# Kernel optimization log

Measured on AMD Instinct MI355X. Metric: run time of the kernel, lower is better.

Reference implementation:

```python
import jax, jax.numpy as jnp
import numpy as np

W_BIT = 4
OUT_F = 11008
IN_F = 4096
K = 16


def unpack_sign(q_bytes):
    """q_bytes: [n_bytes] int32 holding uint8 values. Little-endian bit order.
    Returns float32 signs in {-1, +1} of shape [OUT_F, IN_F]."""
    bits = (q_bytes[:, None] >> jnp.arange(8, dtype=q_bytes.dtype)) & 1  # [n_bytes, 8]
    signs = (2 * bits - 1).astype(jnp.float32)
    return signs.reshape(OUT_F, IN_F)


def setup_inputs() -> dict:
    key = jax.random.key(0)
    k0, k1, k2, k3 = jax.random.split(key, 4)
    x = jax.random.normal(k0, (4, 2048, IN_F), dtype=jnp.float32)
    # packed sign bits: one byte stores 8 signs; OUT_F*IN_F//8 bytes per bit-plane
    qweight = jax.random.randint(k1, (W_BIT, OUT_F * IN_F // 8), 0, 256, dtype=jnp.int32)
    u = jax.random.normal(k2, (W_BIT, OUT_F, K), dtype=jnp.float32) * 0.05
    vt = jax.random.normal(k3, (W_BIT, K, IN_F), dtype=jnp.float32) * 0.05
    return {"x": x, "qweight": qweight, "u": u, "vt": vt}


def reference(x, qweight, u, vt):
    # Reconstruct full weight: w = sum_i sign_i * (u_i @ vt_i), then GEMM x @ w.T.
    # Loop over the small fixed w_bit count to avoid holding all [OUT,IN] bit-planes at once.
    w = jnp.zeros((OUT_F, IN_F), dtype=x.dtype)
    for i in range(W_BIT):
        signs = unpack_sign(qweight[i])            # [OUT_F, IN_F]
        w = w + signs * (u[i] @ vt[i])             # rank-K reconstruction masked by signs
    return x @ w.T                                  # [B, S, OUT_F]
```

## Files before the change

### kernel.cpp

```cpp
#include <hip/hip_runtime.h>
#include <hip/hip_bf16.h>

#define W_BIT 4
#define OUT_F 11008
#define IN_F 4096
#define KRANK 16
#define M_DIM 8192
#define QW_PLANE (OUT_F * IN_F / 8)

#define N_DIM OUT_F
#define K_DIM IN_F
#define NT 64
#define NBN 43

typedef __attribute__((ext_vector_type(8))) short short8;
typedef __attribute__((ext_vector_type(4))) float f32x4;

__device__ __forceinline__ short f2bf(float f) {
    union { float f; unsigned u; } v;
    v.f = f;
    unsigned r = v.u + 0x7fffu + ((v.u >> 16) & 1u);
    return (short)(r >> 16);
}

__device__ __forceinline__ void async16(void* lds, const void* g) {
    __builtin_amdgcn_global_load_lds(
        (const __attribute__((address_space(1))) unsigned int*)g,
        (__attribute__((address_space(3))) unsigned int*)lds,
        16, 0, 0);
}

#define BAR() __builtin_amdgcn_s_barrier()
#define SBAR0() __builtin_amdgcn_sched_barrier(0)
#define LGKM(n) do { asm volatile("s_waitcnt lgkmcnt(" #n ")" ::: "memory"); \
                     __builtin_amdgcn_sched_barrier(0); } while (0)
#define VMC(n) do { asm volatile("s_waitcnt vmcnt(" #n ")" ::: "memory"); \
                    __builtin_amdgcn_sched_barrier(0); } while (0)
#define PRIO1() __builtin_amdgcn_s_setprio(1)
#define PRIO0() __builtin_amdgcn_s_setprio(0)

__global__ __launch_bounds__(256) void convert_x_kernel(
    const float* __restrict__ x, short* __restrict__ xb) {
    int tid = blockIdx.x * blockDim.x + threadIdx.x;
    int stride = gridDim.x * blockDim.x;
    const int n8 = (M_DIM * IN_F) / 8;
    for (int i = tid; i < n8; i += stride) {
        f32x4 a = ((const f32x4*)x)[2 * i];
        f32x4 b = ((const f32x4*)x)[2 * i + 1];
        short8 o;
        o[0] = f2bf(a[0]); o[1] = f2bf(a[1]); o[2] = f2bf(a[2]); o[3] = f2bf(a[3]);
        o[4] = f2bf(b[0]); o[5] = f2bf(b[1]); o[6] = f2bf(b[2]); o[7] = f2bf(b[3]);
        ((short8*)xb)[i] = o;
    }
}

__global__ __launch_bounds__(256) void reconstruct_w_kernel(
    const int* __restrict__ qw, const float* __restrict__ u,
    const float* __restrict__ vt, short* __restrict__ wb) {
    __shared__ float vts[W_BIT][KRANK][128];
    __shared__ float us[W_BIT][KRANK][64];

    const int t = threadIdx.x;
    const int o0 = blockIdx.y * 64;
    const int c0 = blockIdx.x * 128;

    for (int idx = t; idx < W_BIT * KRANK * 128; idx += 256) {
        int i = idx >> 11;
        int rem = idx & 2047;
        int k = rem >> 7;
        int c = rem & 127;
        vts[i][k][c] = vt[(i * KRANK + k) * IN_F + c0 + c];
    }
    for (int idx = t; idx < W_BIT * KRANK * 64; idx += 256) {
        int i = idx >> 10;
        int rem = idx & 1023;
        int o = rem >> 4;
        int k = rem & 15;
        us[i][k][o] = u[((size_t)i * OUT_F + o0 + o) * KRANK + k];
    }
    __syncthreads();

    const int to = (t >> 4) * 4;
    const int tc = (t & 15) * 8;

    float wacc[4][8];
#pragma unroll
    for (int r = 0; r < 4; ++r)
#pragma unroll
        for (int c = 0; c < 8; ++c) wacc[r][c] = 0.f;

#pragma unroll
    for (int i = 0; i < W_BIT; ++i) {
        float dot[4][8];
#pragma unroll
        for (int r = 0; r < 4; ++r)
#pragma unroll
            for (int c = 0; c < 8; ++c) dot[r][c] = 0.f;

#pragma unroll
        for (int k = 0; k < KRANK; ++k) {
            f32x4 uv = *(const f32x4*)&us[i][k][to];
            f32x4 v0 = *(const f32x4*)&vts[i][k][tc];
            f32x4 v1 = *(const f32x4*)&vts[i][k][tc + 4];
#pragma unroll
            for (int r = 0; r < 4; ++r) {
#pragma unroll
                for (int c = 0; c < 4; ++c) {
                    dot[r][c]     += uv[r] * v0[c];
                    dot[r][c + 4] += uv[r] * v1[c];
                }
            }
        }
#pragma unroll
        for (int r = 0; r < 4; ++r) {
            unsigned byte = (unsigned)qw[i * QW_PLANE + (((o0 + to + r) * IN_F + c0 + tc) >> 3)];
#pragma unroll
            for (int c = 0; c < 8; ++c) {
                wacc[r][c] += ((byte >> c) & 1u) ? dot[r][c] : -dot[r][c];
            }
        }
    }

#pragma unroll
    for (int r = 0; r < 4; ++r) {
        short8 o8;
#pragma unroll
        for (int c = 0; c < 8; ++c) o8[c] = f2bf(wacc[r][c]);
        *(short8*)&wb[(size_t)(o0 + to + r) * IN_F + c0 + tc] = o8;
    }
}

__global__ __launch_bounds__(512, 2) void gemm256_kernel(
    const short* __restrict__ A, const short* __restrict__ B, float* __restrict__ C) {
    extern __shared__ short lds[];

    const int t = threadIdx.x;
    const int lane = t & 63, wid = t >> 6;
    const int wr = wid >> 2, wc = wid & 3;
    const int fr = lane & 15, fq = lane >> 4;

    const int bid = blockIdx.x;
    const int cpx = gridDim.x >> 3;
    const int swz = (bid & 7) * cpx + (bid >> 3);
    const int bm = swz / NBN, bn = swz % NBN;
    const long row0 = (long)bm * 256, col0 = (long)bn * 256;

    const int srow_b = t >> 3;
    const int scol = (((t & 7) ^ ((t >> 3) & 7)) << 3);
    const short* gA = A + (row0 + srow_b) * K_DIM + scol;
    const short* gB = B + (col0 + srow_b) * K_DIM + scol;
    const int ldst = t * 8;

    const int arow = (wr * 128 + fr) * 64;
    const int brow = (wc * 64 + fr) * 64;
    const int cswz = (fr & 7) << 3;
    const int colk0  = (fq << 3) ^ cswz;
    const int colk32 = (32 | (fq << 3)) ^ cswz;

    f32x4 acc[8][4];
#pragma unroll
    for (int m = 0; m < 8; ++m)
#pragma unroll
        for (int n = 0; n < 4; ++n) acc[m][n] = (f32x4)0.f;

    short8 af[4][4], bf[2][4];

#define STAGE4(gp, base, ktcol)                                        \
    _Pragma("unroll") for (int l = 0; l < 4; ++l)                      \
        async16(&lds[(base) + ldst + l * 4096],                        \
                (gp) + (size_t)l * 64 * K_DIM + (ktcol))

#define LDA4(j, base, mh, colk)                                        \
    _Pragma("unroll") for (int m = 0; m < 4; ++m)                      \
        af[j][m] = *(const short8*)&lds[(base) + arow + (mh) * 4096 + m * 1024 + (colk)]

#define LDB4(j, base, colk)                                            \
    _Pragma("unroll") for (int n = 0; n < 4; ++n)                      \
        bf[j][n] = *(const short8*)&lds[(base) + 16384 + brow + n * 1024 + (colk)]

#define MFQ(j, jb, mbase)                                              \
    _Pragma("unroll") for (int m = 0; m < 4; ++m)                      \
        _Pragma("unroll") for (int n = 0; n < 4; ++n)                  \
            acc[(mbase) + m][n] = __builtin_amdgcn_mfma_f32_16x16x32_bf16( \
                af[j][m], bf[jb][n], acc[(mbase) + m][n], 0, 0, 0)

    STAGE4(gA, 0, 0);
    STAGE4(gB, 16384, 0);
    STAGE4(gB, 32768 + 16384, 64);
    VMC(4);
    BAR();
    LDA4(0, 0, 0, colk0);
    LDB4(0, 0, colk0);

    for (int g = 0; g < NT; ++g) {
        const int cur = (g & 1) * 32768;
        const int oth = 32768 - cur;
        const bool h1 = (g + 1 < NT);
        const bool h2 = (g + 2 < NT);

        if (h1) STAGE4(gA, oth, (size_t)(g + 1) * 64);
        LDA4(1, cur, 1, colk0);
        BAR();
        LGKM(4);
        PRIO1(); MFQ(0, 0, 0); PRIO0();
        SBAR0();
        BAR();

        LDA4(2, cur, 0, colk32);
        LDB4(1, cur, colk32);
        BAR();
        LGKM(8);
        PRIO1(); MFQ(1, 0, 4); PRIO0();
        SBAR0();
        BAR();

        LDA4(3, cur, 1, colk32);
        BAR();
        LGKM(4);
        PRIO1(); MFQ(2, 1, 0); PRIO0();
        SBAR0();
        BAR();

        if (h2) STAGE4(gB, cur + 16384, (size_t)(g + 2) * 64);
        if (h2) { VMC(4); } else { VMC(0); }
        BAR();
        if (h1) {
            LDA4(0, oth, 0, colk0);
            LDB4(0, oth, colk0);
            LGKM(8);
        } else {
            LGKM(0);
        }
        PRIO1(); MFQ(3, 1, 4); PRIO0();
        SBAR0();
        BAR();
    }

#pragma unroll
    for (int m = 0; m < 8; ++m) {
#pragma unroll
        for (int n = 0; n < 4; ++n) {
            f32x4 v = acc[m][n];
            long r0 = row0 + wr * 128 + m * 16 + fq * 4;
            long cc = col0 + wc * 64 + n * 16 + fr;
#pragma unroll
            for (int jj = 0; jj < 4; ++jj)
                C[(size_t)(r0 + jj) * N_DIM + cc] = v[jj];
        }
    }
#undef STAGE4
#undef LDA4
#undef LDB4
#undef MFQ
}

extern "C" void kernel_launch(void* const* d_in, const int* in_sizes, int n_in,
                              void* d_out, int out_size, void* d_ws, size_t ws_size,
                              hipStream_t stream) {
    const float* x  = (const float*)d_in[0];
    const int*   qw = (const int*)d_in[1];
    const float* u  = (const float*)d_in[2];
    const float* vt = (const float*)d_in[3];
    float* out = (float*)d_out;

    const size_t wb_bytes = (size_t)OUT_F * IN_F * 2;
    short* wb = (short*)d_ws;
    short* xb = (short*)((char*)d_ws + wb_bytes);

    (void)hipFuncSetAttribute((const void*)gemm256_kernel,
                              hipFuncAttributeMaxDynamicSharedMemorySize, 131072);

    hipLaunchKernelGGL(convert_x_kernel, dim3(2048), dim3(256), 0, stream, x, xb);
    hipLaunchKernelGGL(reconstruct_w_kernel, dim3(IN_F / 128, OUT_F / 64), dim3(256), 0, stream,
                       qw, u, vt, wb);
    hipLaunchKernelGGL(gemm256_kernel, dim3((M_DIM / 256) * (N_DIM / 256)), dim3(512), 131072,
                       stream, xb, wb, out);
}
```

Baseline: 901.0 us.

## Restructure GEMM main loop into 4-stage k32 LDS ring pipeline

Replaces the double-buffered 64-wide K tile schedule with a four-slot ring of 32-wide K slices for A and B, prefetching up to three slices ahead with a new XOR swizzle for the LDS layout. The loop is manually unrolled over four slots, with an explicit epilogue, and waits with full lgkmcnt(0) before each MFMA quarter. The aim is to hide global latency better through deeper prefetch. In exchange it adds more barriers per K step and gives up partial LDS-wait overlap.

```diff
diff --git a/kernel.cpp b/kernel.cpp
--- a/kernel.cpp
+++ b/kernel.cpp
@@ -9,7 +9,7 @@
 #define QW_PLANE (OUT_F * IN_F / 8)
 
 #define N_DIM OUT_F
-#define K_DIM IN_F
+#define K_DIM 4096
 #define NT 64
 #define NBN 43
 
@@ -23,16 +23,15 @@
     return (short)(r >> 16);
 }
 
-__device__ __forceinline__ void async16(void* lds, const void* g) {
+__device__ __forceinline__ void async16(void* lds_p, const void* g) {
     __builtin_amdgcn_global_load_lds(
         (const __attribute__((address_space(1))) unsigned int*)g,
-        (__attribute__((address_space(3))) unsigned int*)lds,
+        (__attribute__((address_space(3))) unsigned int*)lds_p,
         16, 0, 0);
 }
 
 #define BAR() __builtin_amdgcn_s_barrier()
-#define SBAR0() __builtin_amdgcn_sched_barrier(0)
-#define LGKM(n) do { asm volatile("s_waitcnt lgkmcnt(" #n ")" ::: "memory"); \
+#define LGKM0() do { asm volatile("s_waitcnt lgkmcnt(0)" ::: "memory"); \
                      __builtin_amdgcn_sched_barrier(0); } while (0)
 #define VMC(n) do { asm volatile("s_waitcnt vmcnt(" #n ")" ::: "memory"); \
                     __builtin_amdgcn_sched_barrier(0); } while (0)
@@ -141,21 +140,21 @@
 
     const int bid = blockIdx.x;
     const int cpx = gridDim.x >> 3;
-    const int swz = (bid & 7) * cpx + (bid >> 3);
-    const int bm = swz / NBN, bn = swz % NBN;
+    const int swzb = (bid & 7) * cpx + (bid >> 3);
+    const int bm = swzb / NBN, bn = swzb % NBN;
     const long row0 = (long)bm * 256, col0 = (long)bn * 256;
 
-    const int srow_b = t >> 3;
-    const int scol = (((t & 7) ^ ((t >> 3) & 7)) << 3);
-    const short* gA = A + (row0 + srow_b) * K_DIM + scol;
-    const short* gB = B + (col0 + srow_b) * K_DIM + scol;
-    const int ldst = t * 8;
-
-    const int arow = (wr * 128 + fr) * 64;
-    const int brow = (wc * 64 + fr) * 64;
-    const int cswz = (fr & 7) << 3;
-    const int colk0  = (fq << 3) ^ cswz;
-    const int colk32 = (32 | (fq << 3)) ^ cswz;
+    const int colswz = (fq ^ ((fr >> 1) & 3)) * 8;
+    const int aoff = (wr * 128 + fr) * 32 + colswz;
+    const int boff = 32768 + (wc * 64 + fr) * 32 + colswz;
+
+    const int srow = t >> 2;
+    const int sswz = (((t & 3) ^ ((srow >> 1) & 3)) << 3);
+    const short* pA0 = A + (row0 + srow) * (size_t)K_DIM + sswz;
+    const short* pA1 = pA0 + (size_t)128 * K_DIM;
+    const short* pB0 = B + (col0 + srow) * (size_t)K_DIM + sswz;
+    const short* pB1 = pB0 + (size_t)128 * K_DIM;
+    const int ldst0 = t * 8;
 
     f32x4 acc[8][4];
 #pragma unroll
@@ -163,78 +162,95 @@
 #pragma unroll
         for (int n = 0; n < 4; ++n) acc[m][n] = (f32x4)0.f;
 
-    short8 af[4][4], bf[2][4];
-
-#define STAGE4(gp, base, ktcol)                                        \
-    _Pragma("unroll") for (int l = 0; l < 4; ++l)                      \
-        async16(&lds[(base) + ldst + l * 4096],                        \
-                (gp) + (size_t)l * 64 * K_DIM + (ktcol))
-
-#define LDA4(j, base, mh, colk)                                        \
+    short8 af[4], bf0[4], bf1[4];
+
+#define STG(P0, P1, SLOT, OFFB) do {                                   \
+    async16(&lds[(SLOT) + ldst0], (const char*)(P0) + (OFFB));         \
+    async16(&lds[(SLOT) + 4096 + ldst0], (const char*)(P1) + (OFFB));  \
+} while (0)
+
+#define RDA(KSLOT, MH) do {                                            \
     _Pragma("unroll") for (int m = 0; m < 4; ++m)                      \
-        af[j][m] = *(const short8*)&lds[(base) + arow + (mh) * 4096 + m * 1024 + (colk)]
-
-#define LDB4(j, base, colk)                                            \
+        af[m] = *(const short8*)&lds[(KSLOT) + ((MH) * 4 + m) * 512 + aoff]; \
+} while (0)
+
+#define RDB(DST, KSLOT) do {                                           \
     _Pragma("unroll") for (int n = 0; n < 4; ++n)                      \
-        bf[j][n] = *(const short8*)&lds[(base) + 16384 + brow + n * 1024 + (colk)]
-
-#define MFQ(j, jb, mbase)                                              \
+        DST[n] = *(const short8*)&lds[(KSLOT) + n * 512 + boff];       \
+} while (0)
+
+#define MFQ(BF, MH) do {                                               \
     _Pragma("unroll") for (int m = 0; m < 4; ++m)                      \
         _Pragma("unroll") for (int n = 0; n < 4; ++n)                  \
-            acc[(mbase) + m][n] = __builtin_amdgcn_mfma_f32_16x16x32_bf16( \
-                af[j][m], bf[jb][n], acc[(mbase) + m][n], 0, 0, 0)
-
-    STAGE4(gA, 0, 0);
-    STAGE4(gB, 16384, 0);
-    STAGE4(gB, 32768 + 16384, 64);
-    VMC(4);
+            acc[(MH) * 4 + m][n] = __builtin_amdgcn_mfma_f32_16x16x32_bf16( \
+                af[m], BF[n], acc[(MH) * 4 + m][n], 0, 0, 0);          \
+} while (0)
+
+#define MMA(BF, MH) do { PRIO1(); MFQ(BF, MH); PRIO0(); } while (0)
+
+    STG(pA0, pA1, 0,     0);
+    STG(pB0, pB1, 32768, 0);
+    STG(pA0, pA1, 8192,  64);
+    STG(pB0, pB1, 40960, 64);
+    STG(pA0, pA1, 16384, 128);
+    STG(pB0, pB1, 49152, 128);
+    VMC(8);
     BAR();
-    LDA4(0, 0, 0, colk0);
-    LDB4(0, 0, colk0);
-
-    for (int g = 0; g < NT; ++g) {
-        const int cur = (g & 1) * 32768;
-        const int oth = 32768 - cur;
-        const bool h1 = (g + 1 < NT);
-        const bool h2 = (g + 2 < NT);
-
-        if (h1) STAGE4(gA, oth, (size_t)(g + 1) * 64);
-        LDA4(1, cur, 1, colk0);
-        BAR();
-        LGKM(4);
-        PRIO1(); MFQ(0, 0, 0); PRIO0();
-        SBAR0();
-        BAR();
-
-        LDA4(2, cur, 0, colk32);
-        LDB4(1, cur, colk32);
-        BAR();
-        LGKM(8);
-        PRIO1(); MFQ(1, 0, 4); PRIO0();
-        SBAR0();
-        BAR();
-
-        LDA4(3, cur, 1, colk32);
-        BAR();
-        LGKM(4);
-        PRIO1(); MFQ(2, 1, 0); PRIO0();
-        SBAR0();
-        BAR();
-
-        if (h2) STAGE4(gB, cur + 16384, (size_t)(g + 2) * 64);
-        if (h2) { VMC(4); } else { VMC(0); }
-        BAR();
-        if (h1) {
-            LDA4(0, oth, 0, colk0);
-            LDB4(0, oth, colk0);
-            LGKM(8);
-        } else {
-            LGKM(0);
-        }
-        PRIO1(); MFQ(3, 1, 4); PRIO0();
-        SBAR0();
-        BAR();
-    }
+
+    for (int it = 0; it < 31; ++it) {
+        RDB(bf0, 0); RDA(0, 0);
+        STG(pA0, pA1, 24576, 192);
+        BAR(); LGKM0(); MMA(bf0, 0); BAR();
+        RDA(0, 1);
+        VMC(6);
+        STG(pB0, pB1, 57344, 192);
+        BAR(); LGKM0(); MMA(bf0, 1); BAR();
+        RDB(bf1, 8192); RDA(8192, 0);
+        STG(pA0, pA1, 0, 256);
+        BAR(); LGKM0(); MMA(bf1, 0); BAR();
+        RDA(8192, 1);
+        VMC(6);
+        STG(pB0, pB1, 32768, 256);
+        BAR(); LGKM0(); MMA(bf1, 1); BAR();
+
+        RDB(bf0, 16384); RDA(16384, 0);
+        STG(pA0, pA1, 8192, 320);
+        BAR(); LGKM0(); MMA(bf0, 0); BAR();
+        RDA(16384, 1);
+        VMC(6);
+        STG(pB0, pB1, 40960, 320);
+        BAR(); LGKM0(); MMA(bf0, 1); BAR();
+        RDB(bf1, 24576); RDA(24576, 0);
+        STG(pA0, pA1, 16384, 384);
+        BAR(); LGKM0(); MMA(bf1, 0); BAR();
+        RDA(24576, 1);
+        VMC(6);
+        STG(pB0, pB1, 49152, 384);
+        BAR(); LGKM0(); MMA(bf1, 1); BAR();
+
+        pA0 += 128; pA1 += 128; pB0 += 128; pB1 += 128;
+    }
+
+    RDB(bf0, 0); RDA(0, 0);
+    STG(pA0, pA1, 24576, 192);
+    BAR(); LGKM0(); MMA(bf0, 0); BAR();
+    RDA(0, 1);
+    VMC(2);
+    STG(pB0, pB1, 57344, 192);
+    BAR(); LGKM0(); MMA(bf0, 1); BAR();
+    RDB(bf1, 8192); RDA(8192, 0);
+    BAR(); LGKM0(); MMA(bf1, 0); BAR();
+    RDA(8192, 1);
+    VMC(0);
+    BAR(); LGKM0(); MMA(bf1, 1); BAR();
+    RDB(bf0, 16384); RDA(16384, 0);
+    BAR(); LGKM0(); MMA(bf0, 0); BAR();
+    RDA(16384, 1);
+    BAR(); LGKM0(); MMA(bf0, 1); BAR();
+    RDB(bf1, 24576); RDA(24576, 0);
+    BAR(); LGKM0(); MMA(bf1, 0); BAR();
+    RDA(24576, 1);
+    BAR(); LGKM0(); MMA(bf1, 1); BAR();
 
 #pragma unroll
     for (int m = 0; m < 8; ++m) {
@@ -248,10 +264,11 @@
                 C[(size_t)(r0 + jj) * N_DIM + cc] = v[jj];
         }
     }
-#undef STAGE4
-#undef LDA4
-#undef LDB4
+#undef STG
+#undef RDA
+#undef RDB
 #undef MFQ
+#undef MMA
 }
 
 extern "C" void kernel_launch(void* const* d_in, const int* in_sizes, int n_in,
```

Measured after the change: 904.7 us. About the same (+0.4%).
